# Performance work log

Hardware: AMD Instinct MI355X
Metric: run time of the kernel (lower is better)

The kernel has to match this reference:

```python
import jax, jax.numpy as jnp
import numpy as np

B, L, D_MODEL = 2, 2048, 1024
N_HEADS, D_K = 16, 64  # d_v == d_k (required by the output*q epilogue)


def setup_inputs() -> dict:
    key = jax.random.key(0)
    ks = jax.random.split(key, 8)
    # xavier_normal std for [d_model, d_k] fan: sqrt(2/(d_model+d_k))
    std = float(np.sqrt(2.0 / (D_MODEL + D_K)))
    std_p = float(np.sqrt(1.0 / (N_HEADS * D_K)))  # nn.Linear default ~ U(-1/sqrt(fan_in),..); normal approx ok for a baseline
    return {
        "q": jax.random.normal(ks[0], (B, L, D_MODEL), jnp.float32),
        "k": jax.random.normal(ks[1], (B, L, D_MODEL), jnp.float32),
        "v": jax.random.normal(ks[2], (B, L, D_MODEL), jnp.float32),
        "w_qs": jax.random.normal(ks[3], (N_HEADS, D_MODEL, D_K), jnp.float32) * std,
        "w_ks": jax.random.normal(ks[4], (N_HEADS, D_MODEL, D_K), jnp.float32) * std,
        "w_vs": jax.random.normal(ks[5], (N_HEADS, D_MODEL, D_K), jnp.float32) * std,
        "w_proj": jax.random.normal(ks[6], (D_MODEL, N_HEADS * D_K), jnp.float32) * std_p,
        "b_proj": jnp.zeros((D_MODEL,), jnp.float32),
    }


def reference(q, k, v, w_qs, w_ks, w_vs, w_proj, b_proj):
    # Per-head projections: [h, B, L, d_k]
    qh = jnp.einsum("bld,hdk->hblk", q, w_qs)
    kh = jnp.einsum("bld,hdk->hblk", k, w_ks)
    vh = jnp.einsum("bld,hdk->hblk", v, w_vs)
    # UNscaled attention (no 1/sqrt(d_k)), dropout is identity at eval
    attn = jax.nn.softmax(jnp.einsum("hblk,hbmk->hblm", qh, kh), axis=-1)
    # attn @ V with elementwise *q epilogue
    out = jnp.einsum("hblm,hbmk->hblk", attn, vh) * qh
    # torch.cat(torch.split(outputs, mb_size, 0), -1): heads concat on last dim
    out = out.transpose(1, 2, 0, 3).reshape(q.shape[0], q.shape[1], -1)  # [B, L, h*d_k]
    return out @ w_proj.T + b_proj
```

## Files before the change

kernel.cpp:

```cpp
#include <hip/hip_runtime.h>

#define B_ 2
#define L_ 2048
#define DM 1024
#define H_ 16
#define DK 64
#define ROWS (B_*L_)
#define BK 32
#define LDT 40

typedef _Float16 f16x8 __attribute__((ext_vector_type(8)));
typedef float    f32x4 __attribute__((ext_vector_type(4)));
typedef unsigned short us8 __attribute__((ext_vector_type(8)));
typedef unsigned short us4v __attribute__((ext_vector_type(4)));

__device__ __forceinline__ unsigned short f2h(float f) {
    _Float16 h = (_Float16)f;
    return __builtin_bit_cast(unsigned short, h);
}
__device__ __forceinline__ float h2f(unsigned short u) {
    return (float)__builtin_bit_cast(_Float16, u);
}
__device__ __forceinline__ f16x8 ld8h(const unsigned short* p) {
    return *reinterpret_cast<const f16x8*>(p);
}
__device__ __forceinline__ us8 cvt_us8(float4 a, float4 b) {
    us8 u;
    u[0] = f2h(a.x); u[1] = f2h(a.y); u[2] = f2h(a.z); u[3] = f2h(a.w);
    u[4] = f2h(b.x); u[5] = f2h(b.y); u[6] = f2h(b.z); u[7] = f2h(b.w);
    return u;
}

#define MFMA(a, b, c) __builtin_amdgcn_mfma_f32_16x16x32_f16((a), (b), (c), 0, 0, 0)

__global__ __launch_bounds__(256) void kcvt(
    const float* __restrict__ src, unsigned short* __restrict__ dst)
{
    size_t i = ((size_t)blockIdx.x * 256 + threadIdx.x) * 8;
    const float4* s4 = (const float4*)(src + i);
    *(us8*)(dst + i) = cvt_us8(s4[0], s4[1]);
}

__global__ __launch_bounds__(256) void k0_transpose_w(
    const float* __restrict__ wq,
    const float* __restrict__ wk,
    const float* __restrict__ wv,
    unsigned short* __restrict__ wt)
{
    __shared__ unsigned short tile[64][65];
    int bx = blockIdx.x;
    int which = bx / (H_ * 16);
    int rem   = bx % (H_ * 16);
    int h  = rem >> 4;
    int db = (rem & 15) * 64;
    const float* src = (which == 0) ? wq : (which == 1) ? wk : wv;
    float scale = (which == 1) ? 1.44269504f : 1.0f;

    int t = threadIdx.x;
    int r = t >> 2;
    int c = (t & 3) * 16;
    const float4* sp = (const float4*)(src + ((size_t)(h * DM + db + r)) * DK + c);
    #pragma unroll
    for (int i4 = 0; i4 < 4; i4++) {
        float4 f = sp[i4];
        tile[r][c + i4 * 4 + 0] = f2h(f.x * scale);
        tile[r][c + i4 * 4 + 1] = f2h(f.y * scale);
        tile[r][c + i4 * 4 + 2] = f2h(f.z * scale);
        tile[r][c + i4 * 4 + 3] = f2h(f.w * scale);
    }
    __syncthreads();

    int n   = t >> 2;
    int d16 = (t & 3) * 16;
    __align__(16) unsigned short ov[16];
    #pragma unroll
    for (int i = 0; i < 16; i++) ov[i] = tile[d16 + i][n];
    size_t off = (((size_t)which * H_ + h) * DK + n) * DM + db + d16;
    *(us8*)(wt + off)     = *(us8*)&ov[0];
    *(us8*)(wt + off + 8) = *(us8*)&ov[8];
}

__global__ __launch_bounds__(256) void k1_proj_qkv(
    const float* __restrict__ q,
    const float* __restrict__ k,
    const float* __restrict__ v,
    const unsigned short* __restrict__ wt,
    unsigned short* __restrict__ qh,
    unsigned short* __restrict__ kh,
    unsigned short* __restrict__ vt)
{
    __shared__ __align__(16) unsigned short sA[128 * LDT];
    __shared__ __align__(16) unsigned short sB[128 * LDT];

    int bx = blockIdx.x;
    int which = bx >> 8;
    int rem   = bx & 255;
    int mbase = (rem >> 3) * 128;
    int nbase = (rem & 7) * 128;

    const float* Ag = (which == 0) ? q : (which == 1) ? k : v;
    const unsigned short* Bg = wt + (size_t)which * DM * DM;

    int t = threadIdx.x;
    int wave = t >> 6, lane = t & 63, quad = lane >> 4, l16 = lane & 15;
    int wm = (wave >> 1) * 64, wn = (wave & 1) * 64;

    int ar0 = t >> 2,         ac0 = t & 3;
    int ar1 = (256 + t) >> 2, ac1 = t & 3;
    const float* pA0 = Ag + (size_t)(mbase + ar0) * DM + ac0 * 8;
    const float* pA1 = Ag + (size_t)(mbase + ar1) * DM + ac1 * 8;
    const unsigned short* pB0 = Bg + (size_t)(nbase + ar0) * DM + ac0 * 8;
    const unsigned short* pB1 = Bg + (size_t)(nbase + ar1) * DM + ac1 * 8;
    unsigned short* wA0 = &sA[ar0 * LDT + ac0 * 8];
    unsigned short* wA1 = &sA[ar1 * LDT + ac1 * 8];
    unsigned short* wB0 = &sB[ar0 * LDT + ac0 * 8];
    unsigned short* wB1 = &sB[ar1 * LDT + ac1 * 8];

    f32x4 acc[4][4];
    #pragma unroll
    for (int mi = 0; mi < 4; mi++)
        #pragma unroll
        for (int ni = 0; ni < 4; ni++) acc[mi][ni] = (f32x4)0.0f;

    float4 rA0a = *(const float4*)pA0, rA0b = *(const float4*)(pA0 + 4);
    float4 rA1a = *(const float4*)pA1, rA1b = *(const float4*)(pA1 + 4);
    us8 rB0 = *(const us8*)pB0, rB1 = *(const us8*)pB1;

    for (int step = 0; step < 32; step++) {
        if (step) __syncthreads();
        *(us8*)wA0 = cvt_us8(rA0a, rA0b);
        *(us8*)wA1 = cvt_us8(rA1a, rA1b);
        *(us8*)wB0 = rB0; *(us8*)wB1 = rB1;
        __syncthreads();
        if (step < 31) {
            pA0 += BK; pA1 += BK; pB0 += BK; pB1 += BK;
            rA0a = *(const float4*)pA0; rA0b = *(const float4*)(pA0 + 4);
            rA1a = *(const float4*)pA1; rA1b = *(const float4*)(pA1 + 4);
            rB0 = *(const us8*)pB0; rB1 = *(const us8*)pB1;
        }
        f16x8 aF[4], bF[4];
        #pragma unroll
        for (int mi = 0; mi < 4; mi++)
            aF[mi] = *(const f16x8*)&sA[(wm + mi * 16 + l16) * LDT + quad * 8];
        #pragma unroll
        for (int ni = 0; ni < 4; ni++)
            bF[ni] = *(const f16x8*)&sB[(wn + ni * 16 + l16) * LDT + quad * 8];
        #pragma unroll
        for (int mi = 0; mi < 4; mi++)
            #pragma unroll
            for (int ni = 0; ni < 4; ni++)
                acc[mi][ni] = MFMA(aF[mi], bF[ni], acc[mi][ni]);
    }

    int h = (nbase >> 6) + (wave & 1);
    if (which < 2) {
        unsigned short* OUT = ((which == 0) ? qh : kh) + (size_t)h * ROWS * DK;
        #pragma unroll
        for (int mi = 0; mi < 4; mi++)
            #pragma unroll
            for (int ni = 0; ni < 4; ni++)
                #pragma unroll
                for (int r = 0; r < 4; r++) {
                    int row = mbase + wm + mi * 16 + quad * 4 + r;
                    OUT[(size_t)row * DK + ni * 16 + l16] = f2h(acc[mi][ni][r]);
                }
    } else {
        unsigned short* OUT = vt + (size_t)h * DK * ROWS;
        #pragma unroll
        for (int mi = 0; mi < 4; mi++)
            #pragma unroll
            for (int ni = 0; ni < 4; ni++) {
                int dk   = ni * 16 + l16;
                int rowb = mbase + wm + mi * 16 + quad * 4;
                us4v pk;
                pk[0] = f2h(acc[mi][ni][0]); pk[1] = f2h(acc[mi][ni][1]);
                pk[2] = f2h(acc[mi][ni][2]); pk[3] = f2h(acc[mi][ni][3]);
                *(us4v*)(OUT + (size_t)dk * ROWS + rowb) = pk;
            }
    }
}

__global__ __launch_bounds__(256) void k2_attn(
    const unsigned short* __restrict__ qh,
    const unsigned short* __restrict__ kh,
    const unsigned short* __restrict__ vt,
    unsigned short* __restrict__ x2)
{
    __shared__ __align__(16) unsigned short ktile[64][72];
    __shared__ __align__(16) unsigned short vtile[64][72];
    __shared__ __align__(16) unsigned short pld[4][16][72];

    int bx = blockIdx.x;
    int xcd = bx & 7;
    int loc = bx >> 3;
    int hb  = xcd * 4 + (loc >> 5);
    int qt  = loc & 31;
    int h = hb >> 1, b = hb & 1;
    int qbase = qt * 64;

    const unsigned short* qhp = qh + ((size_t)h * ROWS + b * L_) * DK;
    const unsigned short* khp = kh + ((size_t)h * ROWS + b * L_) * DK;
    const unsigned short* vtp = vt + (size_t)h * DK * ROWS + b * L_;

    int wave = threadIdx.x >> 6, lane = threadIdx.x & 63;
    int quad = lane >> 4, l16 = lane & 15;
    int t = threadIdx.x;

    int qrow = qbase + wave * 16 + l16;
    f16x8 qb0 = ld8h(qhp + (size_t)qrow * DK + quad * 8);
    f16x8 qb1 = ld8h(qhp + (size_t)qrow * DK + 32 + quad * 8);

    float m_i = -1e30f, l_i = 0.0f;
    f32x4 o[4];
    #pragma unroll
    for (int nt = 0; nt < 4; nt++) o[nt] = (f32x4)0.0f;

    for (int kt = 0; kt < 32; kt++) {
        int kb = kt * 64;
        {
            const unsigned short* kg = khp + (size_t)kb * DK;
            #pragma unroll
            for (int i = 0; i < 2; i++) {
                int c = i * 256 + t;
                int key = c >> 3, ch = (c & 7) * 8;
                *(us8*)&ktile[key][ch] = *(const us8*)(kg + c * 8);
            }
            #pragma unroll
            for (int i = 0; i < 2; i++) {
                int c = i * 256 + t;
                int dk = c >> 3, ch = (c & 7) * 8;
                *(us8*)&vtile[dk][ch] = *(const us8*)(vtp + (size_t)dk * ROWS + kb + ch);
            }
        }
        __syncthreads();

        f32x4 s[4];
        #pragma unroll
        for (int nt = 0; nt < 4; nt++) s[nt] = (f32x4)0.0f;
        __builtin_amdgcn_s_setprio(1);
        #pragma unroll
        for (int nt = 0; nt < 4; nt++) {
            f16x8 ka0 = *(const f16x8*)&ktile[nt * 16 + l16][quad * 8];
            f16x8 ka1 = *(const f16x8*)&ktile[nt * 16 + l16][32 + quad * 8];
            s[nt] = MFMA(ka0, qb0, s[nt]);
            s[nt] = MFMA(ka1, qb1, s[nt]);
        }
        __builtin_amdgcn_s_setprio(0);

        float pm[4];
        #pragma unroll
        for (int nt = 0; nt < 4; nt++) {
            float a = fmaxf(s[nt][0], s[nt][1]);
            float c2 = fmaxf(s[nt][2], s[nt][3]);
            pm[nt] = fmaxf(a, c2);
        }
        float mx = fmaxf(fmaxf(pm[0], pm[1]), fmaxf(pm[2], pm[3]));
        mx = fmaxf(mx, __shfl_xor(mx, 16));
        mx = fmaxf(mx, __shfl_xor(mx, 32));

        if (!__all(mx - m_i <= 11.0f)) {
            float mnew  = fmaxf(m_i, mx);
            float alpha = __builtin_amdgcn_exp2f(m_i - mnew);
            l_i *= alpha;
            #pragma unroll
            for (int r = 0; r < 4; r++) {
                float av = __shfl(alpha, quad * 4 + r);
                #pragma unroll
                for (int nt = 0; nt < 4; nt++) o[nt][r] *= av;
            }
            m_i = mnew;
        }

        float ps[4];
        #pragma unroll
        for (int nt = 0; nt < 4; nt++) {
            float e0 = __builtin_amdgcn_exp2f(s[nt][0] - m_i);
            float e1 = __builtin_amdgcn_exp2f(s[nt][1] - m_i);
            float e2 = __builtin_amdgcn_exp2f(s[nt][2] - m_i);
            float e3 = __builtin_amdgcn_exp2f(s[nt][3] - m_i);
            s[nt][0] = e0; s[nt][1] = e1; s[nt][2] = e2; s[nt][3] = e3;
            ps[nt] = (e0 + e1) + (e2 + e3);
        }
        float rs = (ps[0] + ps[1]) + (ps[2] + ps[3]);
        rs += __shfl_xor(rs, 16);
        rs += __shfl_xor(rs, 32);
        l_i += rs;

        #pragma unroll
        for (int nt = 0; nt < 4; nt++) {
            us4v pk;
            pk[0] = f2h(s[nt][0]); pk[1] = f2h(s[nt][1]);
            pk[2] = f2h(s[nt][2]); pk[3] = f2h(s[nt][3]);
            *(us4v*)&pld[wave][l16][nt * 16 + quad * 4] = pk;
        }

        __builtin_amdgcn_s_setprio(1);
        #pragma unroll
        for (int kk = 0; kk < 2; kk++) {
            f16x8 pa = *(const f16x8*)&pld[wave][l16][kk * 32 + quad * 8];
            #pragma unroll
            for (int nt = 0; nt < 4; nt++) {
                f16x8 vb = *(const f16x8*)&vtile[nt * 16 + l16][kk * 32 + quad * 8];
                o[nt] = MFMA(pa, vb, o[nt]);
            }
        }
        __builtin_amdgcn_s_setprio(0);
        __syncthreads();
    }

    float linv = 1.0f / l_i;
    #pragma unroll
    for (int r = 0; r < 4; r++) {
        float lv = __shfl(linv, quad * 4 + r);
        int row = qbase + wave * 16 + quad * 4 + r;
        #pragma unroll
        for (int nt = 0; nt < 4; nt++) {
            int col = nt * 16 + l16;
            float qv = h2f(qhp[(size_t)row * DK + col]);
            float val = o[nt][r] * lv * qv;
            x2[((size_t)b * L_ + row) * DM + h * DK + col] = f2h(val);
        }
    }
}

__global__ __launch_bounds__(256) void k3_out_proj(
    const unsigned short* __restrict__ x2,
    const unsigned short* __restrict__ wph,
    const float* __restrict__ bias,
    float* __restrict__ out)
{
    __shared__ __align__(16) unsigned short sA[128 * LDT];
    __shared__ __align__(16) unsigned short sB[128 * LDT];

    int bx = blockIdx.x;
    int mbase = (bx >> 3) * 128;
    int nbase = (bx & 7) * 128;

    int t = threadIdx.x;
    int wave = t >> 6, lane = t & 63, quad = lane >> 4, l16 = lane & 15;
    int wm = (wave >> 1) * 64, wn = (wave & 1) * 64;

    int ar0 = t >> 2,         ac0 = t & 3;
    int ar1 = (256 + t) >> 2, ac1 = t & 3;
    const unsigned short* pA0 = x2 + (size_t)(mbase + ar0) * DM + ac0 * 8;
    const unsigned short* pA1 = x2 + (size_t)(mbase + ar1) * DM + ac1 * 8;
    const unsigned short* pB0 = wph + (size_t)(nbase + ar0) * DM + ac0 * 8;
    const unsigned short* pB1 = wph + (size_t)(nbase + ar1) * DM + ac1 * 8;
    unsigned short* wA0 = &sA[ar0 * LDT + ac0 * 8];
    unsigned short* wA1 = &sA[ar1 * LDT + ac1 * 8];
    unsigned short* wB0 = &sB[ar0 * LDT + ac0 * 8];
    unsigned short* wB1 = &sB[ar1 * LDT + ac1 * 8];

    f32x4 acc[4][4];
    #pragma unroll
    for (int mi = 0; mi < 4; mi++)
        #pragma unroll
        for (int ni = 0; ni < 4; ni++) acc[mi][ni] = (f32x4)0.0f;

    us8 rA0 = *(const us8*)pA0, rA1 = *(const us8*)pA1;
    us8 rB0 = *(const us8*)pB0, rB1 = *(const us8*)pB1;

    for (int step = 0; step < 32; step++) {
        if (step) __syncthreads();
        *(us8*)wA0 = rA0; *(us8*)wA1 = rA1;
        *(us8*)wB0 = rB0; *(us8*)wB1 = rB1;
        __syncthreads();
        if (step < 31) {
            pA0 += BK; pA1 += BK; pB0 += BK; pB1 += BK;
            rA0 = *(const us8*)pA0; rA1 = *(const us8*)pA1;
            rB0 = *(const us8*)pB0; rB1 = *(const us8*)pB1;
        }
        f16x8 aF[4], bF[4];
        #pragma unroll
        for (int mi = 0; mi < 4; mi++)
            aF[mi] = *(const f16x8*)&sA[(wm + mi * 16 + l16) * LDT + quad * 8];
        #pragma unroll
        for (int ni = 0; ni < 4; ni++)
            bF[ni] = *(const f16x8*)&sB[(wn + ni * 16 + l16) * LDT + quad * 8];
        #pragma unroll
        for (int mi = 0; mi < 4; mi++)
            #pragma unroll
            for (int ni = 0; ni < 4; ni++)
                acc[mi][ni] = MFMA(aF[mi], bF[ni], acc[mi][ni]);
    }

    float bv[4];
    #pragma unroll
    for (int ni = 0; ni < 4; ni++) bv[ni] = bias[nbase + wn + ni * 16 + l16];

    #pragma unroll
    for (int mi = 0; mi < 4; mi++)
        #pragma unroll
        for (int ni = 0; ni < 4; ni++)
            #pragma unroll
            for (int r = 0; r < 4; r++) {
                int row = mbase + wm + mi * 16 + quad * 4 + r;
                int col = nbase + wn + ni * 16 + l16;
                out[(size_t)row * DM + col] = acc[mi][ni][r] + bv[ni];
            }
}

extern "C" void kernel_launch(void* const* d_in, const int* in_sizes, int n_in,
                              void* d_out, int out_size, void* d_ws, size_t ws_size,
                              hipStream_t stream)
{
    const float* q     = (const float*)d_in[0];
    const float* k     = (const float*)d_in[1];
    const float* v     = (const float*)d_in[2];
    const float* wqs   = (const float*)d_in[3];
    const float* wks   = (const float*)d_in[4];
    const float* wvs   = (const float*)d_in[5];
    const float* wproj = (const float*)d_in[6];
    const float* bproj = (const float*)d_in[7];
    float* out = (float*)d_out;

    char* ws = (char*)d_ws;
    #define MB (size_t)(1024 * 1024)
    unsigned short* wt  = (unsigned short*)(ws);
    unsigned short* wph = (unsigned short*)(ws + 6  * MB);
    unsigned short* qh  = (unsigned short*)(ws + 8  * MB);
    unsigned short* kh  = (unsigned short*)(ws + 16 * MB);
    unsigned short* vt  = (unsigned short*)(ws + 24 * MB);
    unsigned short* x2  = (unsigned short*)(ws + 32 * MB);

    kcvt<<<dim3((DM * DM) / (256 * 8)), dim3(256), 0, stream>>>(wproj, wph);
    k0_transpose_w<<<dim3(3 * H_ * 16), dim3(256), 0, stream>>>(wqs, wks, wvs, wt);

    k1_proj_qkv<<<dim3(3 * 32 * 8), dim3(256), 0, stream>>>(q, k, v, wt, qh, kh, vt);
    k2_attn<<<dim3(H_ * B_ * 32), dim3(256), 0, stream>>>(qh, kh, vt, x2);
    k3_out_proj<<<dim3(32 * 8), dim3(256), 0, stream>>>(x2, wph, bproj, out);
}
```

Before: 260.7 us.

## Pre-convert QKV inputs to fp16 and use direct global-to-LDS loads in GEMMs

Adds a kernel that converts q, k and v activations to fp16 in workspace. A new projection GEMM then loads those fp16 tiles straight into LDS with global_load_lds and no register staging. The output projection moves to the same direct-LDS load scheme without padding, and both GEMMs raise wave priority around the MFMA block. This costs an extra conversion pass and 24MB of workspace traffic. It also drops the register prefetch overlap, and the unpadded LDS layout may cause bank conflicts.

```diff
diff --git a/kernel.cpp b/kernel.cpp
--- a/kernel.cpp
+++ b/kernel.cpp
@@ -33,12 +33,31 @@
 
 #define MFMA(a, b, c) __builtin_amdgcn_mfma_f32_16x16x32_f16((a), (b), (c), 0, 0, 0)
 
+#define AS1 __attribute__((address_space(1)))
+#define AS3 __attribute__((address_space(3)))
+__device__ __forceinline__ void glds16(const void* g, void* l) {
+    __builtin_amdgcn_global_load_lds((const AS1 unsigned int*)g,
+                                     (AS3 unsigned int*)l, 16, 0, 0);
+}
+
 __global__ __launch_bounds__(256) void kcvt(
     const float* __restrict__ src, unsigned short* __restrict__ dst)
 {
     size_t i = ((size_t)blockIdx.x * 256 + threadIdx.x) * 8;
     const float4* s4 = (const float4*)(src + i);
     *(us8*)(dst + i) = cvt_us8(s4[0], s4[1]);
+}
+
+__global__ __launch_bounds__(256) void kcvt3(
+    const float* __restrict__ q, const float* __restrict__ k,
+    const float* __restrict__ v, unsigned short* __restrict__ dst)
+{
+    int bx = blockIdx.x;
+    int which = bx >> 11, rem = bx & 2047;
+    const float* src = (which == 0) ? q : (which == 1) ? k : v;
+    size_t i = ((size_t)rem * 256 + threadIdx.x) * 8;
+    const float4* s4 = (const float4*)(src + i);
+    *(us8*)(dst + (size_t)which * ROWS * DM + i) = cvt_us8(s4[0], s4[1]);
 }
 
 __global__ __launch_bounds__(256) void k0_transpose_w(
@@ -78,6 +97,95 @@
     size_t off = (((size_t)which * H_ + h) * DK + n) * DM + db + d16;
     *(us8*)(wt + off)     = *(us8*)&ov[0];
     *(us8*)(wt + off + 8) = *(us8*)&ov[8];
+}
+
+__global__ __launch_bounds__(256) void k1_proj_fp16(
+    const unsigned short* __restrict__ qkvh,
+    const unsigned short* __restrict__ wt,
+    unsigned short* __restrict__ qh,
+    unsigned short* __restrict__ kh,
+    unsigned short* __restrict__ vt)
+{
+    __shared__ __align__(16) unsigned short sA[128 * BK];
+    __shared__ __align__(16) unsigned short sB[128 * BK];
+
+    int bx = blockIdx.x;
+    int which = bx >> 8;
+    int rem   = bx & 255;
+    int mbase = (rem >> 3) * 128;
+    int nbase = (rem & 7) * 128;
+
+    const unsigned short* Ag = qkvh + (size_t)which * ROWS * DM;
+    const unsigned short* Bg = wt + (size_t)which * DM * DM;
+
+    int t = threadIdx.x;
+    int wave = t >> 6, lane = t & 63, quad = lane >> 4, l16 = lane & 15;
+    int wm = (wave >> 1) * 64, wn = (wave & 1) * 64;
+
+    const unsigned short* gA0 = Ag + (size_t)(mbase + (t >> 2)) * DM + (t & 3) * 8;
+    const unsigned short* gA1 = gA0 + (size_t)64 * DM;
+    const unsigned short* gB0 = Bg + (size_t)(nbase + (t >> 2)) * DM + (t & 3) * 8;
+    const unsigned short* gB1 = gB0 + (size_t)64 * DM;
+    unsigned short* lA0 = &sA[(size_t)t * 8];
+    unsigned short* lA1 = &sA[(size_t)(256 + t) * 8];
+    unsigned short* lB0 = &sB[(size_t)t * 8];
+    unsigned short* lB1 = &sB[(size_t)(256 + t) * 8];
+
+    f32x4 acc[4][4];
+    #pragma unroll
+    for (int mi = 0; mi < 4; mi++)
+        #pragma unroll
+        for (int ni = 0; ni < 4; ni++) acc[mi][ni] = (f32x4)0.0f;
+
+    for (int step = 0; step < 32; step++) {
+        if (step) __syncthreads();
+        glds16(gA0, lA0); glds16(gA1, lA1);
+        glds16(gB0, lB0); glds16(gB1, lB1);
+        gA0 += BK; gA1 += BK; gB0 += BK; gB1 += BK;
+        __syncthreads();
+
+        f16x8 aF[4], bF[4];
+        #pragma unroll
+        for (int mi = 0; mi < 4; mi++)
+            aF[mi] = *(const f16x8*)&sA[(wm + mi * 16 + l16) * BK + quad * 8];
+        #pragma unroll
+        for (int ni = 0; ni < 4; ni++)
+            bF[ni] = *(const f16x8*)&sB[(wn + ni * 16 + l16) * BK + quad * 8];
+        __builtin_amdgcn_s_setprio(1);
+        #pragma unroll
+        for (int mi = 0; mi < 4; mi++)
+            #pragma unroll
+            for (int ni = 0; ni < 4; ni++)
+                acc[mi][ni] = MFMA(aF[mi], bF[ni], acc[mi][ni]);
+        __builtin_amdgcn_s_setprio(0);
+    }
+
+    int h = (nbase >> 6) + (wave & 1);
+    if (which < 2) {
+        unsigned short* OUT = ((which == 0) ? qh : kh) + (size_t)h * ROWS * DK;
+        #pragma unroll
+        for (int mi = 0; mi < 4; mi++)
+            #pragma unroll
+            for (int ni = 0; ni < 4; ni++)
+                #pragma unroll
+                for (int r = 0; r < 4; r++) {
+                    int row = mbase + wm + mi * 16 + quad * 4 + r;
+                    OUT[(size_t)row * DK + ni * 16 + l16] = f2h(acc[mi][ni][r]);
+                }
+    } else {
+        unsigned short* OUT = vt + (size_t)h * DK * ROWS;
+        #pragma unroll
+        for (int mi = 0; mi < 4; mi++)
+            #pragma unroll
+            for (int ni = 0; ni < 4; ni++) {
+                int dk   = ni * 16 + l16;
+                int rowb = mbase + wm + mi * 16 + quad * 4;
+                us4v pk;
+                pk[0] = f2h(acc[mi][ni][0]); pk[1] = f2h(acc[mi][ni][1]);
+                pk[2] = f2h(acc[mi][ni][2]); pk[3] = f2h(acc[mi][ni][3]);
+                *(us4v*)(OUT + (size_t)dk * ROWS + rowb) = pk;
+            }
+    }
 }
 
 __global__ __launch_bounds__(256) void k1_proj_qkv(
@@ -329,8 +437,8 @@
     const float* __restrict__ bias,
     float* __restrict__ out)
 {
-    __shared__ __align__(16) unsigned short sA[128 * LDT];
-    __shared__ __align__(16) unsigned short sB[128 * LDT];
+    __shared__ __align__(16) unsigned short sA[128 * BK];
+    __shared__ __align__(16) unsigned short sB[128 * BK];
 
     int bx = blockIdx.x;
     int mbase = (bx >> 3) * 128;
@@ -340,48 +448,42 @@
     int wave = t >> 6, lane = t & 63, quad = lane >> 4, l16 = lane & 15;
     int wm = (wave >> 1) * 64, wn = (wave & 1) * 64;
 
-    int ar0 = t >> 2,         ac0 = t & 3;
-    int ar1 = (256 + t) >> 2, ac1 = t & 3;
-    const unsigned short* pA0 = x2 + (size_t)(mbase + ar0) * DM + ac0 * 8;
-    const unsigned short* pA1 = x2 + (size_t)(mbase + ar1) * DM + ac1 * 8;
-    const unsigned short* pB0 = wph + (size_t)(nbase + ar0) * DM + ac0 * 8;
-    const unsigned short* pB1 = wph + (size_t)(nbase + ar1) * DM + ac1 * 8;
-    unsigned short* wA0 = &sA[ar0 * LDT + ac0 * 8];
-    unsigned short* wA1 = &sA[ar1 * LDT + ac1 * 8];
-    unsigned short* wB0 = &sB[ar0 * LDT + ac0 * 8];
-    unsigned short* wB1 = &sB[ar1 * LDT + ac1 * 8];
+    const unsigned short* gA0 = x2 + (size_t)(mbase + (t >> 2)) * DM + (t & 3) * 8;
+    const unsigned short* gA1 = gA0 + (size_t)64 * DM;
+    const unsigned short* gB0 = wph + (size_t)(nbase + (t >> 2)) * DM + (t & 3) * 8;
+    const unsigned short* gB1 = gB0 + (size_t)64 * DM;
+    unsigned short* lA0 = &sA[(size_t)t * 8];
+    unsigned short* lA1 = &sA[(size_t)(256 + t) * 8];
+    unsigned short* lB0 = &sB[(size_t)t * 8];
+    unsigned short* lB1 = &sB[(size_t)(256 + t) * 8];
 
     f32x4 acc[4][4];
     #pragma unroll
     for (int mi = 0; mi < 4; mi++)
         #pragma unroll
         for (int ni = 0; ni < 4; ni++) acc[mi][ni] = (f32x4)0.0f;
-
-    us8 rA0 = *(const us8*)pA0, rA1 = *(const us8*)pA1;
-    us8 rB0 = *(const us8*)pB0, rB1 = *(const us8*)pB1;
 
     for (int step = 0; step < 32; step++) {
         if (step) __syncthreads();
-        *(us8*)wA0 = rA0; *(us8*)wA1 = rA1;
-        *(us8*)wB0 = rB0; *(us8*)wB1 = rB1;
+        glds16(gA0, lA0); glds16(gA1, lA1);
+        glds16(gB0, lB0); glds16(gB1, lB1);
+        gA0 += BK; gA1 += BK; gB0 += BK; gB1 += BK;
         __syncthreads();
-        if (step < 31) {
-            pA0 += BK; pA1 += BK; pB0 += BK; pB1 += BK;
-            rA0 = *(const us8*)pA0; rA1 = *(const us8*)pA1;
-            rB0 = *(const us8*)pB0; rB1 = *(const us8*)pB1;
-        }
+
         f16x8 aF[4], bF[4];
         #pragma unroll
         for (int mi = 0; mi < 4; mi++)
-            aF[mi] = *(const f16x8*)&sA[(wm + mi * 16 + l16) * LDT + quad * 8];
+            aF[mi] = *(const f16x8*)&sA[(wm + mi * 16 + l16) * BK + quad * 8];
         #pragma unroll
         for (int ni = 0; ni < 4; ni++)
-            bF[ni] = *(const f16x8*)&sB[(wn + ni * 16 + l16) * LDT + quad * 8];
+            bF[ni] = *(const f16x8*)&sB[(wn + ni * 16 + l16) * BK + quad * 8];
+        __builtin_amdgcn_s_setprio(1);
         #pragma unroll
         for (int mi = 0; mi < 4; mi++)
             #pragma unroll
             for (int ni = 0; ni < 4; ni++)
                 acc[mi][ni] = MFMA(aF[mi], bF[ni], acc[mi][ni]);
+        __builtin_amdgcn_s_setprio(0);
     }
 
     float bv[4];
@@ -416,17 +518,23 @@
 
     char* ws = (char*)d_ws;
     #define MB (size_t)(1024 * 1024)
-    unsigned short* wt  = (unsigned short*)(ws);
-    unsigned short* wph = (unsigned short*)(ws + 6  * MB);
-    unsigned short* qh  = (unsigned short*)(ws + 8  * MB);
-    unsigned short* kh  = (unsigned short*)(ws + 16 * MB);
-    unsigned short* vt  = (unsigned short*)(ws + 24 * MB);
-    unsigned short* x2  = (unsigned short*)(ws + 32 * MB);
+    unsigned short* wt   = (unsigned short*)(ws);
+    unsigned short* wph  = (unsigned short*)(ws + 6  * MB);
+    unsigned short* qh   = (unsigned short*)(ws + 8  * MB);
+    unsigned short* kh   = (unsigned short*)(ws + 16 * MB);
+    unsigned short* vt   = (unsigned short*)(ws + 24 * MB);
+    unsigned short* x2   = (unsigned short*)(ws + 32 * MB);
+    unsigned short* qkvh = (unsigned short*)(ws + 32 * MB);
 
     kcvt<<<dim3((DM * DM) / (256 * 8)), dim3(256), 0, stream>>>(wproj, wph);
     k0_transpose_w<<<dim3(3 * H_ * 16), dim3(256), 0, stream>>>(wqs, wks, wvs, wt);
 
-    k1_proj_qkv<<<dim3(3 * 32 * 8), dim3(256), 0, stream>>>(q, k, v, wt, qh, kh, vt);
+    if (ws_size >= 56 * MB) {
+        kcvt3<<<dim3(3 * 2048), dim3(256), 0, stream>>>(q, k, v, qkvh);
+        k1_proj_fp16<<<dim3(3 * 32 * 8), dim3(256), 0, stream>>>(qkvh, wt, qh, kh, vt);
+    } else {
+        k1_proj_qkv<<<dim3(3 * 32 * 8), dim3(256), 0, stream>>>(q, k, v, wt, qh, kh, vt);
+    }
     k2_attn<<<dim3(H_ * B_ * 32), dim3(256), 0, stream>>>(qh, kh, vt, x2);
     k3_out_proj<<<dim3(32 * 8), dim3(256), 0, stream>>>(x2, wph, bproj, out);
 }
```

Result: faster. 255.4 us (-2.0%).
